# Kernel tuning notes

Measured on AMD Instinct MI355X. Metric: run time of the kernel, lower is better.

Reference implementation:

```python
import jax, jax.numpy as jnp
import numpy as np

N_NODES = 100000


def gcn_conv(x, W, b, src, dst, n_nodes):
    """PyG-style GCNConv: out = D^-1/2 (A+I) D^-1/2 (x W) + b.
    Self-loops handled analytically: self-loop norm = 1/deg[i]."""
    xw = x @ W                                    # [N, F_out]
    ones = jnp.ones_like(dst, dtype=xw.dtype)
    deg = jax.ops.segment_sum(ones, dst, num_segments=n_nodes) + 1.0  # A + I in-degree
    dinv_sqrt = jax.lax.rsqrt(deg)
    norm_e = dinv_sqrt[src] * dinv_sqrt[dst]      # [E]
    msg = xw[src] * norm_e[:, None]               # gather + scale  [E, F_out]
    agg = jax.ops.segment_sum(msg, dst, num_segments=n_nodes)  # scatter-add
    agg = agg + xw / deg[:, None]                 # self-loop contribution
    return agg + b


def setup_inputs() -> dict:
    key = jax.random.key(0)
    k1, k2, k3, k4 = jax.random.split(key, 4)
    N, E = N_NODES, 6400000
    x = jax.random.normal(k1, (N, 1), dtype=jnp.float32)
    edge_index = jax.random.randint(k2, (2, E), 0, N, dtype=jnp.int64)
    W1 = jax.random.normal(k3, (1, 16), dtype=jnp.float32) * (1.0 / np.sqrt(1))
    b1 = jnp.zeros((16,), dtype=jnp.float32)
    W2 = jax.random.normal(k4, (16, 2), dtype=jnp.float32) * (1.0 / np.sqrt(16))
    b2 = jnp.zeros((2,), dtype=jnp.float32)
    return {"x": x, "edge_index": edge_index, "W1": W1, "b1": b1, "W2": W2, "b2": b2}


def reference(x, edge_index, W1, b1, W2, b2):
    src, dst = edge_index[0], edge_index[1]
    h = gcn_conv(x, W1, b1, src, dst, N_NODES)
    h = jax.nn.relu(h)
    # dropout p=0.5: identity in eval mode (train=self.training; reference runs eval)
    h = gcn_conv(h, W2, b2, src, dst, N_NODES)
    return jax.nn.log_softmax(h, axis=1)
```

## Files before the change

### kernel.cpp

```cpp
#include <hip/hip_runtime.h>
#include <math.h>


#define NB_MAX 512
#define CAP    17408u
#define TILE   4096
#define EPT    16

__global__ __launch_bounds__(512) void k_init(int NB, unsigned* __restrict__ cursor) {
    int b = threadIdx.x;
    if (b < NB) cursor[b] = (unsigned)b * CAP;
}

__global__ __launch_bounds__(256) void k_bin(const int* __restrict__ src,
                                             const int* __restrict__ dst, int E, int NB,
                                             unsigned* __restrict__ cursor,
                                             unsigned* __restrict__ binned) {
    __shared__ unsigned cnt[NB_MAX];
    __shared__ unsigned pfx[NB_MAX];
    __shared__ unsigned lbase[NB_MAX];
    __shared__ unsigned gbase[NB_MAX];
    __shared__ unsigned svals[TILE];
    __shared__ unsigned short sbkt[TILE];

    const int lo = blockIdx.x * TILE;
    const int n  = min(E - lo, TILE);
    const int t  = threadIdx.x;
    const int nq    = n >> 2;
    const int ntail = n - (nq << 2);

    for (int b = t; b < NB_MAX; b += 256) cnt[b] = 0;
    __syncthreads();

    const int4* d4 = (const int4*)(dst + lo);
    const int4* s4 = (const int4*)(src + lo);

    unsigned val[EPT];
    unsigned brk[EPT];

#pragma unroll
    for (int k = 0; k < 4; ++k) {
        const int j = t + (k << 8);
        if (j < nq) {
            int4 d = d4[j];
            int4 s = s4[j];
            {
                unsigned du = (unsigned)d.x, su = (unsigned)s.x;
                unsigned b = du >> 8;
                unsigned r = atomicAdd(&cnt[b], 1u);
                val[k * 4 + 0] = (su << 8) | (du & 255u);
                brk[k * 4 + 0] = (b << 13) | r;
            }
            {
                unsigned du = (unsigned)d.y, su = (unsigned)s.y;
                unsigned b = du >> 8;
                unsigned r = atomicAdd(&cnt[b], 1u);
                val[k * 4 + 1] = (su << 8) | (du & 255u);
                brk[k * 4 + 1] = (b << 13) | r;
            }
            {
                unsigned du = (unsigned)d.z, su = (unsigned)s.z;
                unsigned b = du >> 8;
                unsigned r = atomicAdd(&cnt[b], 1u);
                val[k * 4 + 2] = (su << 8) | (du & 255u);
                brk[k * 4 + 2] = (b << 13) | r;
            }
            {
                unsigned du = (unsigned)d.w, su = (unsigned)s.w;
                unsigned b = du >> 8;
                unsigned r = atomicAdd(&cnt[b], 1u);
                val[k * 4 + 3] = (su << 8) | (du & 255u);
                brk[k * 4 + 3] = (b << 13) | r;
            }
        } else {
            brk[k * 4 + 0] = 0xFFFFFFFFu;
            brk[k * 4 + 1] = 0xFFFFFFFFu;
            brk[k * 4 + 2] = 0xFFFFFFFFu;
            brk[k * 4 + 3] = 0xFFFFFFFFu;
            val[k * 4 + 0] = 0; val[k * 4 + 1] = 0;
            val[k * 4 + 2] = 0; val[k * 4 + 3] = 0;
        }
    }
    unsigned tval = 0, tbrk = 0xFFFFFFFFu;
    if (t < ntail) {
        unsigned du = (unsigned)dst[lo + (nq << 2) + t];
        unsigned su = (unsigned)src[lo + (nq << 2) + t];
        unsigned b = du >> 8;
        unsigned r = atomicAdd(&cnt[b], 1u);
        tval = (su << 8) | (du & 255u);
        tbrk = (b << 13) | r;
    }
    __syncthreads();

    pfx[t]       = cnt[t];
    pfx[t + 256] = cnt[t + 256];
    __syncthreads();
    for (int o = 1; o < NB_MAX; o <<= 1) {
        unsigned v0 = (t >= o) ? pfx[t - o] : 0u;
        unsigned v1 = (t + 256 >= o) ? pfx[t + 256 - o] : 0u;
        __syncthreads();
        if (t >= o) pfx[t] += v0;
        pfx[t + 256] += v1;
        __syncthreads();
    }
    for (int b = t; b < NB_MAX; b += 256) {
        unsigned c = cnt[b];
        lbase[b] = pfx[b] - c;
        gbase[b] = (b < NB && c) ? atomicAdd(&cursor[b], c) : 0u;
    }
    __syncthreads();

#pragma unroll
    for (int k = 0; k < EPT; ++k) {
        if (brk[k] != 0xFFFFFFFFu) {
            unsigned b = brk[k] >> 13, r = brk[k] & 8191u;
            unsigned pos = lbase[b] + r;
            svals[pos] = val[k];
            sbkt[pos]  = (unsigned short)b;
        }
    }
    if (tbrk != 0xFFFFFFFFu) {
        unsigned b = tbrk >> 13, r = tbrk & 8191u;
        unsigned pos = lbase[b] + r;
        svals[pos] = tval;
        sbkt[pos]  = (unsigned short)b;
    }
    __syncthreads();

    for (int j = t; j < n; j += 256) {
        unsigned b = sbkt[j];
        binned[gbase[b] + ((unsigned)j - lbase[b])] = svals[j];
    }
}

__global__ __launch_bounds__(1024) void k_sort(const unsigned* __restrict__ binned,
                                               const unsigned* __restrict__ cursor,
                                               const float* __restrict__ x, int N,
                                               unsigned* __restrict__ sorted,
                                               unsigned* __restrict__ off,
                                               float* __restrict__ deg,
                                               float* __restrict__ dinv,
                                               float* __restrict__ y) {
    __shared__ unsigned hist[256];
    __shared__ unsigned incl[256];
    __shared__ unsigned exS[256];
    __shared__ unsigned rk[256];
    const int t = threadIdx.x;
    const unsigned b   = blockIdx.x;
    const unsigned lo  = b * CAP;
    const unsigned cnt = cursor[b] - lo;
    if (t < 256) { hist[t] = 0; rk[t] = 0; }
    __syncthreads();

    {
        unsigned i = t;
        for (; i + 3072 < cnt; i += 4096) {
            unsigned p0 = binned[lo + i];
            unsigned p1 = binned[lo + i + 1024];
            unsigned p2 = binned[lo + i + 2048];
            unsigned p3 = binned[lo + i + 3072];
            atomicAdd(&hist[p0 & 255u], 1u);
            atomicAdd(&hist[p1 & 255u], 1u);
            atomicAdd(&hist[p2 & 255u], 1u);
            atomicAdd(&hist[p3 & 255u], 1u);
        }
        for (; i < cnt; i += 1024) atomicAdd(&hist[binned[lo + i] & 255u], 1u);
    }
    __syncthreads();

    if (t < 256) incl[t] = hist[t];
    __syncthreads();
    for (int o = 1; o < 256; o <<= 1) {
        unsigned v = 0;
        if (t < 256 && t >= o) v = incl[t - o];
        __syncthreads();
        if (t < 256 && t >= o) incl[t] += v;
        __syncthreads();
    }
    if (t < 256) {
        exS[t] = incl[t] - hist[t];
        const int g = (int)(b << 8) + t;
        if (g < N) {
            float d  = (float)hist[t] + 1.0f;
            float di = rsqrtf(d);
            deg[g]  = d;
            dinv[g] = di;
            y[g]    = x[g] * di;
            off[g]  = lo + exS[t];
        }
    }
    __syncthreads();

    {
        unsigned i = t;
        for (; i + 3072 < cnt; i += 4096) {
            unsigned p0 = binned[lo + i];
            unsigned p1 = binned[lo + i + 1024];
            unsigned p2 = binned[lo + i + 2048];
            unsigned p3 = binned[lo + i + 3072];
            unsigned l0 = p0 & 255u, l1 = p1 & 255u;
            unsigned l2 = p2 & 255u, l3 = p3 & 255u;
            sorted[lo + exS[l0] + atomicAdd(&rk[l0], 1u)] = p0 >> 8;
            sorted[lo + exS[l1] + atomicAdd(&rk[l1], 1u)] = p1 >> 8;
            sorted[lo + exS[l2] + atomicAdd(&rk[l2], 1u)] = p2 >> 8;
            sorted[lo + exS[l3] + atomicAdd(&rk[l3], 1u)] = p3 >> 8;
        }
        for (; i < cnt; i += 1024) {
            unsigned p = binned[lo + i];
            unsigned l = p & 255u;
            sorted[lo + exS[l] + atomicAdd(&rk[l], 1u)] = p >> 8;
        }
    }
}

__global__ __launch_bounds__(256) void k_agg1(const unsigned* __restrict__ sorted,
                                              const unsigned* __restrict__ off,
                                              const float* __restrict__ deg,
                                              const float* __restrict__ dinv,
                                              const float* __restrict__ x,
                                              const float* __restrict__ y,
                                              const float* __restrict__ W1,
                                              const float* __restrict__ b1,
                                              const float* __restrict__ W2, int N,
                                              float* __restrict__ z,
                                              float* __restrict__ zs) {
    const int tid = blockIdx.x * 256 + threadIdx.x;
    const int g   = tid >> 3;
    const int h   = tid & 7;
    if (g >= N) return;
    const float d   = deg[g];
    const int   n   = (int)d - 1;
    const unsigned lo = off[g];
    float acc = 0.0f;
    int i = h;
    for (; i + 8 < n; i += 16) {
        unsigned s0 = sorted[lo + i];
        unsigned s1 = sorted[lo + i + 8];
        acc += y[s0];
        acc += y[s1];
    }
    for (; i < n; i += 8) acc += y[sorted[lo + i]];
    acc += __shfl_xor(acc, 1);
    acc += __shfl_xor(acc, 2);
    acc += __shfl_xor(acc, 4);
    float di  = dinv[g];
    float s1v = fmaf(di, acc, x[g] / d);
    float z0 = 0.0f, z1 = 0.0f;
#pragma unroll
    for (int f = 0; f < 16; ++f) {
        float hh = fmaxf(fmaf(s1v, W1[f], b1[f]), 0.0f);
        z0 = fmaf(hh, W2[2 * f + 0], z0);
        z1 = fmaf(hh, W2[2 * f + 1], z1);
    }
    if (h == 0) {
        ((float2*)z)[g]  = make_float2(z0, z1);
        ((float2*)zs)[g] = make_float2(z0 * di, z1 * di);
    }
}

__global__ __launch_bounds__(256) void k_agg2(const unsigned* __restrict__ sorted,
                                              const unsigned* __restrict__ off,
                                              const float* __restrict__ deg,
                                              const float* __restrict__ dinv,
                                              const float* __restrict__ z,
                                              const float* __restrict__ zs,
                                              const float* __restrict__ b2, int N,
                                              float* __restrict__ out) {
    const int tid = blockIdx.x * 256 + threadIdx.x;
    const int g   = tid >> 3;
    const int h   = tid & 7;
    if (g >= N) return;
    const float d   = deg[g];
    const int   n   = (int)d - 1;
    const unsigned lo = off[g];
    const float2* zs2 = (const float2*)zs;
    float a0 = 0.0f, a1 = 0.0f;
    int i = h;
    for (; i + 8 < n; i += 16) {
        unsigned s0 = sorted[lo + i];
        unsigned s1 = sorted[lo + i + 8];
        float2 v0 = zs2[s0];
        float2 v1 = zs2[s1];
        a0 += v0.x + v1.x;
        a1 += v0.y + v1.y;
    }
    for (; i < n; i += 8) {
        float2 v = zs2[sorted[lo + i]];
        a0 += v.x;
        a1 += v.y;
    }
    a0 += __shfl_xor(a0, 1);
    a0 += __shfl_xor(a0, 2);
    a0 += __shfl_xor(a0, 4);
    a1 += __shfl_xor(a1, 1);
    a1 += __shfl_xor(a1, 2);
    a1 += __shfl_xor(a1, 4);
    if (h == 0) {
        float di   = dinv[g];
        float invd = 1.0f / d;
        float2 zz  = ((const float2*)z)[g];
        float o0 = fmaf(di, a0, zz.x * invd) + b2[0];
        float o1 = fmaf(di, a1, zz.y * invd) + b2[1];
        float m   = fmaxf(o0, o1);
        float lse = m + __logf(__expf(o0 - m) + __expf(o1 - m));
        ((float2*)out)[g] = make_float2(o0 - lse, o1 - lse);
    }
}

extern "C" void kernel_launch(void* const* d_in, const int* in_sizes, int n_in,
                              void* d_out, int out_size, void* d_ws, size_t ws_size,
                              hipStream_t stream) {
    const float* x  = (const float*)d_in[0];
    const int*   ei = (const int*)d_in[1];
    const float* W1 = (const float*)d_in[2];
    const float* b1 = (const float*)d_in[3];
    const float* W2 = (const float*)d_in[4];
    const float* b2 = (const float*)d_in[5];

    const int N = in_sizes[0];
    const int E = in_sizes[1] / 2;
    const int* src = ei;
    const int* dst = ei + E;

    const int NB = (N + 255) >> 8;

    char* p = (char*)d_ws;
    unsigned* binned = (unsigned*)p;  p += ((size_t)NB * CAP + TILE) * 4;
    unsigned* sorted = (unsigned*)p;  p += (size_t)NB * CAP * 4;
    unsigned* off    = (unsigned*)p;  p += (size_t)N * 4;
    float* deg  = (float*)p;          p += (size_t)N * 4;
    float* dinv = (float*)p;          p += (size_t)N * 4;
    float* y    = (float*)p;          p += (size_t)N * 4;
    unsigned* cursor = (unsigned*)p;  p += (size_t)NB_MAX * 4;
    float* z  = (float*)binned;
    float* zs = ((float*)binned) + 2 * (size_t)N;

    const int nb_bin = (E + TILE - 1) / TILE;
    const int nb_agg = (8 * N + 255) / 256;

    k_init <<<1, 512, 0, stream>>>(NB, cursor);
    k_bin  <<<nb_bin, 256, 0, stream>>>(src, dst, E, NB, cursor, binned);
    k_sort <<<NB, 1024, 0, stream>>>(binned, cursor, x, N, sorted, off, deg, dinv, y);
    k_agg1 <<<nb_agg, 256, 0, stream>>>(sorted, off, deg, dinv, x, y, W1, b1, W2, N, z, zs);
    k_agg2 <<<nb_agg, 256, 0, stream>>>(sorted, off, deg, dinv, z, zs, b2, N, (float*)d_out);
}
```

Before: 239.0 us.

## Split sort into degree pass and scatter pass that packs pre-gathered y with indices

The sort kernel is split in two. The first kernel computes degrees, offsets and y. The second scatters the sorted source indices, and when workspace allows it stores each index alongside the gathered y[src] value as a uint2. Layer-1 aggregation can then stream the packed values contiguously instead of doing random gathers, at the cost of an extra kernel launch, a second pass over the binned data and doubled sorted-array traffic in layer 2. The binning kernel also moves to 512 threads with an 8192-edge tile, halving the number of blocks and global cursor atomics.

```diff
diff --git a/kernel.cpp b/kernel.cpp
--- a/kernel.cpp
+++ b/kernel.cpp
@@ -4,7 +4,7 @@
 
 #define NB_MAX 512
 #define CAP    17408u
-#define TILE   4096
+#define TILE   8192
 #define EPT    16
 
 __global__ __launch_bounds__(512) void k_init(int NB, unsigned* __restrict__ cursor) {
@@ -12,7 +12,7 @@
     if (b < NB) cursor[b] = (unsigned)b * CAP;
 }
 
-__global__ __launch_bounds__(256) void k_bin(const int* __restrict__ src,
+__global__ __launch_bounds__(512) void k_bin(const int* __restrict__ src,
                                              const int* __restrict__ dst, int E, int NB,
                                              unsigned* __restrict__ cursor,
                                              unsigned* __restrict__ binned) {
@@ -29,7 +29,7 @@
     const int nq    = n >> 2;
     const int ntail = n - (nq << 2);
 
-    for (int b = t; b < NB_MAX; b += 256) cnt[b] = 0;
+    cnt[t] = 0;
     __syncthreads();
 
     const int4* d4 = (const int4*)(dst + lo);
@@ -40,7 +40,7 @@
 
 #pragma unroll
     for (int k = 0; k < 4; ++k) {
-        const int j = t + (k << 8);
+        const int j = t + (k << 9);
         if (j < nq) {
             int4 d = d4[j];
             int4 s = s4[j];
@@ -73,10 +73,8 @@
                 brk[k * 4 + 3] = (b << 13) | r;
             }
         } else {
-            brk[k * 4 + 0] = 0xFFFFFFFFu;
-            brk[k * 4 + 1] = 0xFFFFFFFFu;
-            brk[k * 4 + 2] = 0xFFFFFFFFu;
-            brk[k * 4 + 3] = 0xFFFFFFFFu;
+            brk[k * 4 + 0] = 0xFFFFFFFFu; brk[k * 4 + 1] = 0xFFFFFFFFu;
+            brk[k * 4 + 2] = 0xFFFFFFFFu; brk[k * 4 + 3] = 0xFFFFFFFFu;
             val[k * 4 + 0] = 0; val[k * 4 + 1] = 0;
             val[k * 4 + 2] = 0; val[k * 4 + 3] = 0;
         }
@@ -92,21 +90,18 @@
     }
     __syncthreads();
 
-    pfx[t]       = cnt[t];
-    pfx[t + 256] = cnt[t + 256];
+    pfx[t] = cnt[t];
     __syncthreads();
     for (int o = 1; o < NB_MAX; o <<= 1) {
-        unsigned v0 = (t >= o) ? pfx[t - o] : 0u;
-        unsigned v1 = (t + 256 >= o) ? pfx[t + 256 - o] : 0u;
+        unsigned v = (t >= o) ? pfx[t - o] : 0u;
         __syncthreads();
-        if (t >= o) pfx[t] += v0;
-        pfx[t + 256] += v1;
+        if (t >= o) pfx[t] += v;
         __syncthreads();
     }
-    for (int b = t; b < NB_MAX; b += 256) {
-        unsigned c = cnt[b];
-        lbase[b] = pfx[b] - c;
-        gbase[b] = (b < NB && c) ? atomicAdd(&cursor[b], c) : 0u;
+    {
+        unsigned c = cnt[t];
+        lbase[t] = pfx[t] - c;
+        gbase[t] = (t < NB && c) ? atomicAdd(&cursor[t], c) : 0u;
     }
     __syncthreads();
 
@@ -127,29 +122,26 @@
     }
     __syncthreads();
 
-    for (int j = t; j < n; j += 256) {
+    for (int j = t; j < n; j += 512) {
         unsigned b = sbkt[j];
         binned[gbase[b] + ((unsigned)j - lbase[b])] = svals[j];
     }
 }
 
-__global__ __launch_bounds__(1024) void k_sort(const unsigned* __restrict__ binned,
-                                               const unsigned* __restrict__ cursor,
-                                               const float* __restrict__ x, int N,
-                                               unsigned* __restrict__ sorted,
-                                               unsigned* __restrict__ off,
-                                               float* __restrict__ deg,
-                                               float* __restrict__ dinv,
-                                               float* __restrict__ y) {
+__global__ __launch_bounds__(1024) void k_sortA(const unsigned* __restrict__ binned,
+                                                const unsigned* __restrict__ cursor,
+                                                const float* __restrict__ x, int N,
+                                                unsigned* __restrict__ off,
+                                                float* __restrict__ deg,
+                                                float* __restrict__ dinv,
+                                                float* __restrict__ y) {
     __shared__ unsigned hist[256];
     __shared__ unsigned incl[256];
-    __shared__ unsigned exS[256];
-    __shared__ unsigned rk[256];
     const int t = threadIdx.x;
     const unsigned b   = blockIdx.x;
     const unsigned lo  = b * CAP;
     const unsigned cnt = cursor[b] - lo;
-    if (t < 256) { hist[t] = 0; rk[t] = 0; }
+    if (t < 256) hist[t] = 0;
     __syncthreads();
 
     {
@@ -178,7 +170,6 @@
         __syncthreads();
     }
     if (t < 256) {
-        exS[t] = incl[t] - hist[t];
         const int g = (int)(b << 8) + t;
         if (g < N) {
             float d  = (float)hist[t] + 1.0f;
@@ -186,34 +177,67 @@
             deg[g]  = d;
             dinv[g] = di;
             y[g]    = x[g] * di;
-            off[g]  = lo + exS[t];
-        }
-    }
-    __syncthreads();
-
-    {
-        unsigned i = t;
-        for (; i + 3072 < cnt; i += 4096) {
-            unsigned p0 = binned[lo + i];
-            unsigned p1 = binned[lo + i + 1024];
-            unsigned p2 = binned[lo + i + 2048];
-            unsigned p3 = binned[lo + i + 3072];
-            unsigned l0 = p0 & 255u, l1 = p1 & 255u;
-            unsigned l2 = p2 & 255u, l3 = p3 & 255u;
-            sorted[lo + exS[l0] + atomicAdd(&rk[l0], 1u)] = p0 >> 8;
-            sorted[lo + exS[l1] + atomicAdd(&rk[l1], 1u)] = p1 >> 8;
-            sorted[lo + exS[l2] + atomicAdd(&rk[l2], 1u)] = p2 >> 8;
-            sorted[lo + exS[l3] + atomicAdd(&rk[l3], 1u)] = p3 >> 8;
-        }
-        for (; i < cnt; i += 1024) {
-            unsigned p = binned[lo + i];
-            unsigned l = p & 255u;
-            sorted[lo + exS[l] + atomicAdd(&rk[l], 1u)] = p >> 8;
-        }
-    }
-}
-
-__global__ __launch_bounds__(256) void k_agg1(const unsigned* __restrict__ sorted,
+            off[g]  = lo + (incl[t] - hist[t]);
+        }
+    }
+}
+
+template <bool WITH_Y>
+__global__ __launch_bounds__(1024) void k_sortB(const unsigned* __restrict__ binned,
+                                                const unsigned* __restrict__ cursor,
+                                                const unsigned* __restrict__ off,
+                                                const float* __restrict__ y, int N,
+                                                uint2* __restrict__ sorted2,
+                                                unsigned* __restrict__ sortedU) {
+    __shared__ unsigned rk[256];
+    __shared__ unsigned offl[256];
+    const int t = threadIdx.x;
+    const unsigned b   = blockIdx.x;
+    const unsigned lo  = b * CAP;
+    const unsigned cnt = cursor[b] - lo;
+    if (t < 256) {
+        rk[t] = 0;
+        const int g = (int)(b << 8) + t;
+        offl[t] = (g < N) ? off[g] : 0u;
+    }
+    __syncthreads();
+
+    unsigned i = t;
+    for (; i + 3072 < cnt; i += 4096) {
+        unsigned p0 = binned[lo + i];
+        unsigned p1 = binned[lo + i + 1024];
+        unsigned p2 = binned[lo + i + 2048];
+        unsigned p3 = binned[lo + i + 3072];
+        unsigned l0 = p0 & 255u, l1 = p1 & 255u, l2 = p2 & 255u, l3 = p3 & 255u;
+        unsigned s0 = p0 >> 8,   s1 = p1 >> 8,   s2 = p2 >> 8,   s3 = p3 >> 8;
+        unsigned q0 = offl[l0] + atomicAdd(&rk[l0], 1u);
+        unsigned q1 = offl[l1] + atomicAdd(&rk[l1], 1u);
+        unsigned q2 = offl[l2] + atomicAdd(&rk[l2], 1u);
+        unsigned q3 = offl[l3] + atomicAdd(&rk[l3], 1u);
+        if (WITH_Y) {
+            sorted2[q0] = make_uint2(s0, __float_as_uint(y[s0]));
+            sorted2[q1] = make_uint2(s1, __float_as_uint(y[s1]));
+            sorted2[q2] = make_uint2(s2, __float_as_uint(y[s2]));
+            sorted2[q3] = make_uint2(s3, __float_as_uint(y[s3]));
+        } else {
+            sortedU[q0] = s0;
+            sortedU[q1] = s1;
+            sortedU[q2] = s2;
+            sortedU[q3] = s3;
+        }
+    }
+    for (; i < cnt; i += 1024) {
+        unsigned p = binned[lo + i];
+        unsigned l = p & 255u, s = p >> 8;
+        unsigned q = offl[l] + atomicAdd(&rk[l], 1u);
+        if (WITH_Y) sorted2[q] = make_uint2(s, __float_as_uint(y[s]));
+        else        sortedU[q] = s;
+    }
+}
+
+template <bool WITH_Y>
+__global__ __launch_bounds__(256) void k_agg1(const uint2* __restrict__ sorted2,
+                                              const unsigned* __restrict__ sortedU,
                                               const unsigned* __restrict__ off,
                                               const float* __restrict__ deg,
                                               const float* __restrict__ dinv,
@@ -234,12 +258,18 @@
     float acc = 0.0f;
     int i = h;
     for (; i + 8 < n; i += 16) {
-        unsigned s0 = sorted[lo + i];
-        unsigned s1 = sorted[lo + i + 8];
-        acc += y[s0];
-        acc += y[s1];
-    }
-    for (; i < n; i += 8) acc += y[sorted[lo + i]];
+        if (WITH_Y) {
+            acc += __uint_as_float(sorted2[lo + i].y);
+            acc += __uint_as_float(sorted2[lo + i + 8].y);
+        } else {
+            unsigned s0 = sortedU[lo + i];
+            unsigned s1 = sortedU[lo + i + 8];
+            acc += y[s0];
+            acc += y[s1];
+        }
+    }
+    for (; i < n; i += 8)
+        acc += WITH_Y ? __uint_as_float(sorted2[lo + i].y) : y[sortedU[lo + i]];
     acc += __shfl_xor(acc, 1);
     acc += __shfl_xor(acc, 2);
     acc += __shfl_xor(acc, 4);
@@ -258,7 +288,9 @@
     }
 }
 
-__global__ __launch_bounds__(256) void k_agg2(const unsigned* __restrict__ sorted,
+template <bool WITH_Y>
+__global__ __launch_bounds__(256) void k_agg2(const uint2* __restrict__ sorted2,
+                                              const unsigned* __restrict__ sortedU,
                                               const unsigned* __restrict__ off,
                                               const float* __restrict__ deg,
                                               const float* __restrict__ dinv,
@@ -277,15 +309,16 @@
     float a0 = 0.0f, a1 = 0.0f;
     int i = h;
     for (; i + 8 < n; i += 16) {
-        unsigned s0 = sorted[lo + i];
-        unsigned s1 = sorted[lo + i + 8];
+        unsigned s0 = WITH_Y ? sorted2[lo + i].x     : sortedU[lo + i];
+        unsigned s1 = WITH_Y ? sorted2[lo + i + 8].x : sortedU[lo + i + 8];
         float2 v0 = zs2[s0];
         float2 v1 = zs2[s1];
         a0 += v0.x + v1.x;
         a1 += v0.y + v1.y;
     }
     for (; i < n; i += 8) {
-        float2 v = zs2[sorted[lo + i]];
+        unsigned s = WITH_Y ? sorted2[lo + i].x : sortedU[lo + i];
+        float2 v = zs2[s];
         a0 += v.x;
         a1 += v.y;
     }
@@ -324,13 +357,21 @@
 
     const int NB = (N + 255) >> 8;
 
+    const size_t binned_b = ((size_t)NB * CAP + TILE) * 4;
+    const size_t node_b   = (size_t)N * 4;
+    const size_t s2_b     = (size_t)NB * CAP * 8;
+    const size_t sU_b     = (size_t)NB * CAP * 4;
+    const size_t fixed_b  = binned_b + 4 * node_b + (size_t)NB_MAX * 4 + 256;
+    const bool with_y = (fixed_b + s2_b) <= ws_size;
+
     char* p = (char*)d_ws;
-    unsigned* binned = (unsigned*)p;  p += ((size_t)NB * CAP + TILE) * 4;
-    unsigned* sorted = (unsigned*)p;  p += (size_t)NB * CAP * 4;
-    unsigned* off    = (unsigned*)p;  p += (size_t)N * 4;
-    float* deg  = (float*)p;          p += (size_t)N * 4;
-    float* dinv = (float*)p;          p += (size_t)N * 4;
-    float* y    = (float*)p;          p += (size_t)N * 4;
+    unsigned* binned = (unsigned*)p;  p += binned_b;
+    uint2*    sorted2 = (uint2*)p;
+    unsigned* sortedU = (unsigned*)p; p += (with_y ? s2_b : sU_b);
+    unsigned* off    = (unsigned*)p;  p += node_b;
+    float* deg  = (float*)p;          p += node_b;
+    float* dinv = (float*)p;          p += node_b;
+    float* y    = (float*)p;          p += node_b;
     unsigned* cursor = (unsigned*)p;  p += (size_t)NB_MAX * 4;
     float* z  = (float*)binned;
     float* zs = ((float*)binned) + 2 * (size_t)N;
@@ -338,9 +379,20 @@
     const int nb_bin = (E + TILE - 1) / TILE;
     const int nb_agg = (8 * N + 255) / 256;
 
-    k_init <<<1, 512, 0, stream>>>(NB, cursor);
-    k_bin  <<<nb_bin, 256, 0, stream>>>(src, dst, E, NB, cursor, binned);
-    k_sort <<<NB, 1024, 0, stream>>>(binned, cursor, x, N, sorted, off, deg, dinv, y);
-    k_agg1 <<<nb_agg, 256, 0, stream>>>(sorted, off, deg, dinv, x, y, W1, b1, W2, N, z, zs);
-    k_agg2 <<<nb_agg, 256, 0, stream>>>(sorted, off, deg, dinv, z, zs, b2, N, (float*)d_out);
-}
+    k_init  <<<1, 512, 0, stream>>>(NB, cursor);
+    k_bin   <<<nb_bin, 512, 0, stream>>>(src, dst, E, NB, cursor, binned);
+    k_sortA <<<NB, 1024, 0, stream>>>(binned, cursor, x, N, off, deg, dinv, y);
+    if (with_y) {
+        k_sortB<true><<<NB, 1024, 0, stream>>>(binned, cursor, off, y, N, sorted2, sortedU);
+        k_agg1<true><<<nb_agg, 256, 0, stream>>>(sorted2, sortedU, off, deg, dinv, x, y,
+                                                 W1, b1, W2, N, z, zs);
+        k_agg2<true><<<nb_agg, 256, 0, stream>>>(sorted2, sortedU, off, deg, dinv, z, zs,
+                                                 b2, N, (float*)d_out);
+    } else {
+        k_sortB<false><<<NB, 1024, 0, stream>>>(binned, cursor, off, y, N, sorted2, sortedU);
+        k_agg1<false><<<nb_agg, 256, 0, stream>>>(sorted2, sortedU, off, deg, dinv, x, y,
+                                                  W1, b1, W2, N, z, zs);
+        k_agg2<false><<<nb_agg, 256, 0, stream>>>(sorted2, sortedU, off, deg, dinv, z, zs,
+                                                  b2, N, (float*)d_out);
+    }
+}
```

New measurement: 228.6 us. -4.4%, faster.

## Fuse layer-1 aggregation into an LDS-resident bucket sort and widen binning tiles

Applied to the files above, without the earlier changes.

Sorting is split into a histogram/degree pass and a second pass. The second pass scatters each bucket's sources into LDS together with their gathered y values, then runs the layer-1 aggregation and the small MLP directly from LDS, so the separate k_agg1 kernel and its re-read of the sorted edge list go away. k_bin now uses 1024-thread blocks over 16K-edge tiles, with the packed rank field widened to 14 bits. The cost is heavy LDS use in k_sortB (about 140KB per block), which limits occupancy to one block per CU. The z/zs buffers also get their own workspace instead of aliasing binned.

```diff
diff --git a/kernel.cpp b/kernel.cpp
--- a/kernel.cpp
+++ b/kernel.cpp
@@ -4,7 +4,7 @@
 
 #define NB_MAX 512
 #define CAP    17408u
-#define TILE   4096
+#define TILE   16384
 #define EPT    16
 
 __global__ __launch_bounds__(512) void k_init(int NB, unsigned* __restrict__ cursor) {
@@ -12,10 +12,10 @@
     if (b < NB) cursor[b] = (unsigned)b * CAP;
 }
 
-__global__ __launch_bounds__(256) void k_bin(const int* __restrict__ src,
-                                             const int* __restrict__ dst, int E, int NB,
-                                             unsigned* __restrict__ cursor,
-                                             unsigned* __restrict__ binned) {
+__global__ __launch_bounds__(1024) void k_bin(const int* __restrict__ src,
+                                              const int* __restrict__ dst, int E, int NB,
+                                              unsigned* __restrict__ cursor,
+                                              unsigned* __restrict__ binned) {
     __shared__ unsigned cnt[NB_MAX];
     __shared__ unsigned pfx[NB_MAX];
     __shared__ unsigned lbase[NB_MAX];
@@ -29,7 +29,7 @@
     const int nq    = n >> 2;
     const int ntail = n - (nq << 2);
 
-    for (int b = t; b < NB_MAX; b += 256) cnt[b] = 0;
+    if (t < NB_MAX) cnt[t] = 0;
     __syncthreads();
 
     const int4* d4 = (const int4*)(dst + lo);
@@ -40,7 +40,7 @@
 
 #pragma unroll
     for (int k = 0; k < 4; ++k) {
-        const int j = t + (k << 8);
+        const int j = t + (k << 10);
         if (j < nq) {
             int4 d = d4[j];
             int4 s = s4[j];
@@ -49,34 +49,32 @@
                 unsigned b = du >> 8;
                 unsigned r = atomicAdd(&cnt[b], 1u);
                 val[k * 4 + 0] = (su << 8) | (du & 255u);
-                brk[k * 4 + 0] = (b << 13) | r;
+                brk[k * 4 + 0] = (b << 14) | r;
             }
             {
                 unsigned du = (unsigned)d.y, su = (unsigned)s.y;
                 unsigned b = du >> 8;
                 unsigned r = atomicAdd(&cnt[b], 1u);
                 val[k * 4 + 1] = (su << 8) | (du & 255u);
-                brk[k * 4 + 1] = (b << 13) | r;
+                brk[k * 4 + 1] = (b << 14) | r;
             }
             {
                 unsigned du = (unsigned)d.z, su = (unsigned)s.z;
                 unsigned b = du >> 8;
                 unsigned r = atomicAdd(&cnt[b], 1u);
                 val[k * 4 + 2] = (su << 8) | (du & 255u);
-                brk[k * 4 + 2] = (b << 13) | r;
+                brk[k * 4 + 2] = (b << 14) | r;
             }
             {
                 unsigned du = (unsigned)d.w, su = (unsigned)s.w;
                 unsigned b = du >> 8;
                 unsigned r = atomicAdd(&cnt[b], 1u);
                 val[k * 4 + 3] = (su << 8) | (du & 255u);
-                brk[k * 4 + 3] = (b << 13) | r;
+                brk[k * 4 + 3] = (b << 14) | r;
             }
         } else {
-            brk[k * 4 + 0] = 0xFFFFFFFFu;
-            brk[k * 4 + 1] = 0xFFFFFFFFu;
-            brk[k * 4 + 2] = 0xFFFFFFFFu;
-            brk[k * 4 + 3] = 0xFFFFFFFFu;
+            brk[k * 4 + 0] = 0xFFFFFFFFu; brk[k * 4 + 1] = 0xFFFFFFFFu;
+            brk[k * 4 + 2] = 0xFFFFFFFFu; brk[k * 4 + 3] = 0xFFFFFFFFu;
             val[k * 4 + 0] = 0; val[k * 4 + 1] = 0;
             val[k * 4 + 2] = 0; val[k * 4 + 3] = 0;
         }
@@ -88,68 +86,63 @@
         unsigned b = du >> 8;
         unsigned r = atomicAdd(&cnt[b], 1u);
         tval = (su << 8) | (du & 255u);
-        tbrk = (b << 13) | r;
-    }
-    __syncthreads();
-
-    pfx[t]       = cnt[t];
-    pfx[t + 256] = cnt[t + 256];
+        tbrk = (b << 14) | r;
+    }
+    __syncthreads();
+
+    if (t < NB_MAX) pfx[t] = cnt[t];
     __syncthreads();
     for (int o = 1; o < NB_MAX; o <<= 1) {
-        unsigned v0 = (t >= o) ? pfx[t - o] : 0u;
-        unsigned v1 = (t + 256 >= o) ? pfx[t + 256 - o] : 0u;
+        unsigned v = 0;
+        if (t < NB_MAX && t >= o) v = pfx[t - o];
         __syncthreads();
-        if (t >= o) pfx[t] += v0;
-        pfx[t + 256] += v1;
+        if (t < NB_MAX && t >= o) pfx[t] += v;
         __syncthreads();
     }
-    for (int b = t; b < NB_MAX; b += 256) {
-        unsigned c = cnt[b];
-        lbase[b] = pfx[b] - c;
-        gbase[b] = (b < NB && c) ? atomicAdd(&cursor[b], c) : 0u;
+    if (t < NB_MAX) {
+        unsigned c = cnt[t];
+        lbase[t] = pfx[t] - c;
+        gbase[t] = (t < NB && c) ? atomicAdd(&cursor[t], c) : 0u;
     }
     __syncthreads();
 
 #pragma unroll
     for (int k = 0; k < EPT; ++k) {
         if (brk[k] != 0xFFFFFFFFu) {
-            unsigned b = brk[k] >> 13, r = brk[k] & 8191u;
+            unsigned b = brk[k] >> 14, r = brk[k] & 16383u;
             unsigned pos = lbase[b] + r;
             svals[pos] = val[k];
             sbkt[pos]  = (unsigned short)b;
         }
     }
     if (tbrk != 0xFFFFFFFFu) {
-        unsigned b = tbrk >> 13, r = tbrk & 8191u;
+        unsigned b = tbrk >> 14, r = tbrk & 16383u;
         unsigned pos = lbase[b] + r;
         svals[pos] = tval;
         sbkt[pos]  = (unsigned short)b;
     }
     __syncthreads();
 
-    for (int j = t; j < n; j += 256) {
+    for (int j = t; j < n; j += 1024) {
         unsigned b = sbkt[j];
         binned[gbase[b] + ((unsigned)j - lbase[b])] = svals[j];
     }
 }
 
-__global__ __launch_bounds__(1024) void k_sort(const unsigned* __restrict__ binned,
-                                               const unsigned* __restrict__ cursor,
-                                               const float* __restrict__ x, int N,
-                                               unsigned* __restrict__ sorted,
-                                               unsigned* __restrict__ off,
-                                               float* __restrict__ deg,
-                                               float* __restrict__ dinv,
-                                               float* __restrict__ y) {
+__global__ __launch_bounds__(1024) void k_sortA(const unsigned* __restrict__ binned,
+                                                const unsigned* __restrict__ cursor,
+                                                const float* __restrict__ x, int N,
+                                                unsigned* __restrict__ off,
+                                                float* __restrict__ deg,
+                                                float* __restrict__ dinv,
+                                                float* __restrict__ y) {
     __shared__ unsigned hist[256];
     __shared__ unsigned incl[256];
-    __shared__ unsigned exS[256];
-    __shared__ unsigned rk[256];
     const int t = threadIdx.x;
     const unsigned b   = blockIdx.x;
     const unsigned lo  = b * CAP;
     const unsigned cnt = cursor[b] - lo;
-    if (t < 256) { hist[t] = 0; rk[t] = 0; }
+    if (t < 256) hist[t] = 0;
     __syncthreads();
 
     {
@@ -178,7 +171,6 @@
         __syncthreads();
     }
     if (t < 256) {
-        exS[t] = incl[t] - hist[t];
         const int g = (int)(b << 8) + t;
         if (g < N) {
             float d  = (float)hist[t] + 1.0f;
@@ -186,8 +178,36 @@
             deg[g]  = d;
             dinv[g] = di;
             y[g]    = x[g] * di;
-            off[g]  = lo + exS[t];
-        }
+            off[g]  = lo + (incl[t] - hist[t]);
+        }
+    }
+}
+
+__global__ __launch_bounds__(1024) void k_sortB(const unsigned* __restrict__ binned,
+                                                const unsigned* __restrict__ cursor,
+                                                const unsigned* __restrict__ off,
+                                                const float* __restrict__ deg,
+                                                const float* __restrict__ dinv,
+                                                const float* __restrict__ x,
+                                                const float* __restrict__ y,
+                                                const float* __restrict__ W1,
+                                                const float* __restrict__ b1,
+                                                const float* __restrict__ W2, int N,
+                                                unsigned* __restrict__ sorted,
+                                                float* __restrict__ z,
+                                                float* __restrict__ zs) {
+    __shared__ unsigned srt[CAP];
+    __shared__ float    yv[CAP];
+    __shared__ unsigned rk[256];
+    __shared__ unsigned offl[256];
+    const int t = threadIdx.x;
+    const unsigned b   = blockIdx.x;
+    const unsigned lo  = b * CAP;
+    const unsigned cnt = cursor[b] - lo;
+    if (t < 256) {
+        rk[t] = 0;
+        const int g = (int)(b << 8) + t;
+        offl[t] = (g < N) ? (off[g] - lo) : 0u;
     }
     __syncthreads();
 
@@ -198,63 +218,56 @@
             unsigned p1 = binned[lo + i + 1024];
             unsigned p2 = binned[lo + i + 2048];
             unsigned p3 = binned[lo + i + 3072];
-            unsigned l0 = p0 & 255u, l1 = p1 & 255u;
-            unsigned l2 = p2 & 255u, l3 = p3 & 255u;
-            sorted[lo + exS[l0] + atomicAdd(&rk[l0], 1u)] = p0 >> 8;
-            sorted[lo + exS[l1] + atomicAdd(&rk[l1], 1u)] = p1 >> 8;
-            sorted[lo + exS[l2] + atomicAdd(&rk[l2], 1u)] = p2 >> 8;
-            sorted[lo + exS[l3] + atomicAdd(&rk[l3], 1u)] = p3 >> 8;
+            unsigned l0 = p0 & 255u, l1 = p1 & 255u, l2 = p2 & 255u, l3 = p3 & 255u;
+            unsigned s0 = p0 >> 8,   s1 = p1 >> 8,   s2 = p2 >> 8,   s3 = p3 >> 8;
+            float y0 = y[s0], y1 = y[s1], y2 = y[s2], y3 = y[s3];
+            unsigned q0 = offl[l0] + atomicAdd(&rk[l0], 1u);
+            unsigned q1 = offl[l1] + atomicAdd(&rk[l1], 1u);
+            unsigned q2 = offl[l2] + atomicAdd(&rk[l2], 1u);
+            unsigned q3 = offl[l3] + atomicAdd(&rk[l3], 1u);
+            srt[q0] = s0; yv[q0] = y0;
+            srt[q1] = s1; yv[q1] = y1;
+            srt[q2] = s2; yv[q2] = y2;
+            srt[q3] = s3; yv[q3] = y3;
         }
         for (; i < cnt; i += 1024) {
             unsigned p = binned[lo + i];
-            unsigned l = p & 255u;
-            sorted[lo + exS[l] + atomicAdd(&rk[l], 1u)] = p >> 8;
-        }
-    }
-}
-
-__global__ __launch_bounds__(256) void k_agg1(const unsigned* __restrict__ sorted,
-                                              const unsigned* __restrict__ off,
-                                              const float* __restrict__ deg,
-                                              const float* __restrict__ dinv,
-                                              const float* __restrict__ x,
-                                              const float* __restrict__ y,
-                                              const float* __restrict__ W1,
-                                              const float* __restrict__ b1,
-                                              const float* __restrict__ W2, int N,
-                                              float* __restrict__ z,
-                                              float* __restrict__ zs) {
-    const int tid = blockIdx.x * 256 + threadIdx.x;
-    const int g   = tid >> 3;
-    const int h   = tid & 7;
-    if (g >= N) return;
-    const float d   = deg[g];
-    const int   n   = (int)d - 1;
-    const unsigned lo = off[g];
-    float acc = 0.0f;
-    int i = h;
-    for (; i + 8 < n; i += 16) {
-        unsigned s0 = sorted[lo + i];
-        unsigned s1 = sorted[lo + i + 8];
-        acc += y[s0];
-        acc += y[s1];
-    }
-    for (; i < n; i += 8) acc += y[sorted[lo + i]];
-    acc += __shfl_xor(acc, 1);
-    acc += __shfl_xor(acc, 2);
-    acc += __shfl_xor(acc, 4);
-    float di  = dinv[g];
-    float s1v = fmaf(di, acc, x[g] / d);
-    float z0 = 0.0f, z1 = 0.0f;
+            unsigned l = p & 255u, s = p >> 8;
+            unsigned q = offl[l] + atomicAdd(&rk[l], 1u);
+            srt[q] = s;
+            yv[q]  = y[s];
+        }
+    }
+    __syncthreads();
+
+    for (unsigned j = t; j < cnt; j += 1024) sorted[lo + j] = srt[j];
+
+    {
+        const int ln = t >> 2;
+        const int h  = t & 3;
+        const int g  = (int)(b << 8) + ln;
+        if (g < N) {
+            const float d  = deg[g];
+            const int   n  = (int)d - 1;
+            const unsigned base = offl[ln];
+            float acc = 0.0f;
+            for (int i = h; i < n; i += 4) acc += yv[base + i];
+            acc += __shfl_xor(acc, 1);
+            acc += __shfl_xor(acc, 2);
+            float di  = dinv[g];
+            float s1v = fmaf(di, acc, x[g] / d);
+            float z0 = 0.0f, z1 = 0.0f;
 #pragma unroll
-    for (int f = 0; f < 16; ++f) {
-        float hh = fmaxf(fmaf(s1v, W1[f], b1[f]), 0.0f);
-        z0 = fmaf(hh, W2[2 * f + 0], z0);
-        z1 = fmaf(hh, W2[2 * f + 1], z1);
-    }
-    if (h == 0) {
-        ((float2*)z)[g]  = make_float2(z0, z1);
-        ((float2*)zs)[g] = make_float2(z0 * di, z1 * di);
+            for (int f = 0; f < 16; ++f) {
+                float hh = fmaxf(fmaf(s1v, W1[f], b1[f]), 0.0f);
+                z0 = fmaf(hh, W2[2 * f + 0], z0);
+                z1 = fmaf(hh, W2[2 * f + 1], z1);
+            }
+            if (h == 0) {
+                ((float2*)z)[g]  = make_float2(z0, z1);
+                ((float2*)zs)[g] = make_float2(z0 * di, z1 * di);
+            }
+        }
     }
 }
 
@@ -331,16 +344,18 @@
     float* deg  = (float*)p;          p += (size_t)N * 4;
     float* dinv = (float*)p;          p += (size_t)N * 4;
     float* y    = (float*)p;          p += (size_t)N * 4;
+    float* z    = (float*)p;          p += (size_t)2 * N * 4;
+    float* zs   = (float*)p;          p += (size_t)2 * N * 4;
     unsigned* cursor = (unsigned*)p;  p += (size_t)NB_MAX * 4;
-    float* z  = (float*)binned;
-    float* zs = ((float*)binned) + 2 * (size_t)N;
 
     const int nb_bin = (E + TILE - 1) / TILE;
     const int nb_agg = (8 * N + 255) / 256;
 
-    k_init <<<1, 512, 0, stream>>>(NB, cursor);
-    k_bin  <<<nb_bin, 256, 0, stream>>>(src, dst, E, NB, cursor, binned);
-    k_sort <<<NB, 1024, 0, stream>>>(binned, cursor, x, N, sorted, off, deg, dinv, y);
-    k_agg1 <<<nb_agg, 256, 0, stream>>>(sorted, off, deg, dinv, x, y, W1, b1, W2, N, z, zs);
-    k_agg2 <<<nb_agg, 256, 0, stream>>>(sorted, off, deg, dinv, z, zs, b2, N, (float*)d_out);
-}
+    k_init  <<<1, 512, 0, stream>>>(NB, cursor);
+    k_bin   <<<nb_bin, 1024, 0, stream>>>(src, dst, E, NB, cursor, binned);
+    k_sortA <<<NB, 1024, 0, stream>>>(binned, cursor, x, N, off, deg, dinv, y);
+    k_sortB <<<NB, 1024, 0, stream>>>(binned, cursor, off, deg, dinv, x, y,
+                                      W1, b1, W2, N, sorted, z, zs);
+    k_agg2  <<<nb_agg, 256, 0, stream>>>(sorted, off, deg, dinv, z, zs, b2, N,
+                                         (float*)d_out);
+}
```

After: 193.2 us. 19.2% less time.
